# Performance work log

Hardware: AMD Instinct MI355X
Metric: run time of the kernel (lower is better)

Reference implementation:

```python
import jax, jax.numpy as jnp
import numpy as np

I_DIM, K_DIM, V_DIM, O_DIM = 64, 64, 32, 64
P, NH, NK = 7, 2, 4
B, H, W = 8, 256, 256


def get_unfold_params_v2(width, kernel_size, num_kernels):
    # exact replica of the torch helper's search
    if width <= kernel_size:
        return width, 1, 1, 1
    if width <= kernel_size + num_kernels:
        return kernel_size, 1, 1, width - kernel_size + 1

    def _sd(nk):
        d = 1
        while True:
            k = (kernel_size - 1) * d + 1
            if (width - k) % (nk - 1) == 0:
                return (width - k) // (nk - 1), d
            d += 1
            if d >= kernel_size:
                return None, d

    while True:
        s, d = _sd(num_kernels)
        if s and s < (kernel_size - 1) * d + 1:
            return kernel_size, s, d, num_kernels
        num_kernels += 1


def conv1x1(x, Wt, b):
    # x: [B,C,H,W], Wt: [O,C]
    return jnp.einsum('oc,bchw->bohw', Wt, x) + b[None, :, None, None]


def to_patches(x, nh, idx, p):
    # x: [B,C,H,W] -> [B, nh, nph*npw, C//nh, p*p] (unfold + rearrange)
    Bs, C, _, _ = x.shape
    hd = C // nh
    npw = idx.shape[0]
    pt = x[:, :, idx][:, :, :, :, idx]          # [B,C,nph,ph,npw,pw]
    pt = pt.reshape(Bs, nh, hd, npw, p, npw, p)
    pt = pt.transpose(0, 1, 3, 5, 2, 4, 6)       # B,nh,nph,npw,hd,ph,pw
    return pt.reshape(Bs, nh, npw * npw, hd, p * p)


def from_patches(o, nh, idx, p, Hh, Ww):
    # o: [B,nh,S,hd,p*p] -> fold (overlap scatter-add) -> [B, nh*hd, H, W]
    Bs, _, _, hd, _ = o.shape
    npw = idx.shape[0]
    o = o.reshape(Bs, nh, npw, npw, hd, p, p)
    o = o.transpose(0, 1, 4, 2, 5, 3, 6)         # B,nh,hd,nph,ph,npw,pw
    o = o.reshape(Bs, nh * hd, npw, p, npw, p)
    out = jnp.zeros((Bs, nh * hd, Hh, Ww), o.dtype)
    return out.at[:, :, idx[:, :, None, None], idx[None, None, :, :]].add(o)


def setup_inputs() -> dict:
    key = jax.random.key(0)
    ks = jax.random.split(key, 8)
    s = 0.05
    return {
        'x1': jax.random.normal(ks[0], (B, I_DIM, H, W), jnp.float32),
        'x2': jax.random.normal(ks[1], (B, I_DIM, H, W), jnp.float32),
        'Wk': jax.random.normal(ks[2], (2 * K_DIM, I_DIM), jnp.float32) * s,
        'bk': jax.random.normal(ks[3], (2 * K_DIM,), jnp.float32) * s,
        'Wv': jax.random.normal(ks[4], (2 * V_DIM, I_DIM), jnp.float32) * s,
        'bv': jax.random.normal(ks[5], (2 * V_DIM,), jnp.float32) * s,
        'Wp': jax.random.normal(ks[6], (O_DIM, 2 * V_DIM), jnp.float32) * s,
        'bp': jax.random.normal(ks[7], (O_DIM,), jnp.float32) * s,
    }


def reference(x1, x2, Wk, bk, Wv, bv, Wp, bp):
    _, _, Hh, Ww = x1.shape
    p, stride, dilation, nkrn = get_unfold_params_v2(Ww, P, NK)
    idx = np.arange(nkrn)[:, None] * stride + np.arange(p)[None, :] * dilation  # [npw,p]

    # grouped 1x1 convs (groups=2): split weights into per-stream halves
    k1 = conv1x1(x1, Wk[:K_DIM], bk[:K_DIM])
    k2 = conv1x1(x2, Wk[K_DIM:], bk[K_DIM:])
    v1 = conv1x1(x1, Wv[:V_DIM], bv[:V_DIM])
    v2 = conv1x1(x2, Wv[V_DIM:], bv[V_DIM:])

    k1p = to_patches(k1, NH, idx, p)  # [B,nh,S,hd_k,pp]
    k2p = to_patches(k2, NH, idx, p)
    v1p = to_patches(v1, NH, idx, p)  # [B,nh,S,hd_v,pp]
    v2p = to_patches(v2, NH, idx, p)

    scale = k1p.shape[-2] ** (-0.5)
    kk = jnp.einsum('bnsdx,bnsdy->bnsxy', k1p * scale, k2p)  # [B,nh,S,pp,pp]
    a1 = jax.nn.softmax(kk, axis=-2)
    o1 = jnp.einsum('bnsxy,bnsdx->bnsdy', a1, v1p)
    a2 = jax.nn.softmax(kk, axis=-1)
    o2 = jnp.einsum('bnsxy,bnsdy->bnsdx', a2, v2p)

    o1 = from_patches(o1, NH, idx, p, Hh, Ww)  # [B,V_DIM,H,W]
    o2 = from_patches(o2, NH, idx, p, Hh, Ww)
    o = jnp.concatenate([o1, o2], axis=1)      # [B,2*V_DIM,H,W]
    return conv1x1(o, Wp, bp)                  # [B,O_DIM,H,W]
```

## Files before the change

### kernel.cpp

```cpp
#include <hip/hip_runtime.h>

#define BB 8
#define HH 256
#define CIN 64
#define NPW 12
#define SPP 144
#define PP 49
#define PDIM 7
#define STRIDE 21
#define DIL 4
#define NS 84

typedef __attribute__((ext_vector_type(8))) short bf16x8;
typedef __attribute__((ext_vector_type(4))) float f32x4;

#define MFMA(a, b, c) __builtin_amdgcn_mfma_f32_16x16x32_bf16((a), (b), (c), 0, 0, 0)

static __device__ __forceinline__ unsigned short f2bf(float f) {
  union { float f; unsigned u; } v; v.f = f;
  unsigned r = (v.u + 0x7fffu + ((v.u >> 16) & 1u)) >> 16;
  return (unsigned short)r;
}
static __device__ __forceinline__ float bf2f(unsigned short h) {
  union { unsigned u; float f; } v; v.u = ((unsigned)h) << 16;
  return v.f;
}
static __device__ __forceinline__ unsigned pk2(float a, float b) {
  return (unsigned)f2bf(a) | ((unsigned)f2bf(b) << 16);
}
static __device__ __forceinline__ int swz(int col, int row) {
  return ((((col >> 3) ^ (row & 7)) & 7) << 3) | (col & 7);
}

__global__ __launch_bounds__(256, 4) void k1_fused(
    const float* __restrict__ x1, const float* __restrict__ x2,
    const float* __restrict__ Wk, const float* __restrict__ bk,
    const float* __restrict__ Wv, const float* __restrict__ bv,
    const float* __restrict__ Wp, float* __restrict__ P)
{
  __shared__ __align__(16) short lds[20480];

  const int tid = threadIdx.x;
  const int lane = tid & 63;
  const int wid = tid >> 6;
  const int l16 = lane & 15;
  const int l4 = lane >> 4;
  const int blk = blockIdx.x;
  const int b  = blk / SPP;
  const int sp = blk % SPP;
  const int pi = sp / NPW, pj = sp % NPW;
  const int h0 = pi * STRIDE, w0 = pj * STRIDE;

  bf16x8 ahi[3][2], alo[3][2];
  float bias[3][4];
  #pragma unroll
  for (int mi = 0; mi < 3; mi++) {
    const int m = wid * 3 + mi;
    const int r0 = m * 16;
    const int rl = r0 + l16;
    const float* wrow = (r0 < 128) ? (Wk + (size_t)rl * 64)
                                   : (Wv + (size_t)(rl - 128) * 64);
    #pragma unroll
    for (int kt = 0; kt < 2; kt++) {
      const float* wp8 = wrow + kt * 32 + l4 * 8;
      float4 wa = *(const float4*)wp8;
      float4 wb = *(const float4*)(wp8 + 4);
      float wf[8] = {wa.x, wa.y, wa.z, wa.w, wb.x, wb.y, wb.z, wb.w};
      #pragma unroll
      for (int j = 0; j < 8; j++) {
        unsigned short h = f2bf(wf[j]);
        ahi[mi][kt][j] = (short)h;
        alo[mi][kt][j] = (short)f2bf(wf[j] - bf2f(h));
      }
    }
    #pragma unroll
    for (int i = 0; i < 4; i++) {
      int rd = r0 + l4 * 4 + i;
      bias[mi][i] = (r0 < 128) ? bk[rd] : bv[rd - 128];
    }
  }
  float4 wpraw[4];
  {
    const float* wprow = Wp + (size_t)(wid * 16 + l16) * 64;
    #pragma unroll
    for (int kt = 0; kt < 2; kt++) {
      wpraw[kt * 2 + 0] = *(const float4*)(wprow + kt * 32 + l4 * 8);
      wpraw[kt * 2 + 1] = *(const float4*)(wprow + kt * 32 + l4 * 8 + 4);
    }
  }

  for (int i = tid; i < 2 * CIN * PP; i += 256) {
    int src = i / (CIN * PP);
    int r = i - src * (CIN * PP);
    int c = r / PP, t = r - c * PP;
    int ph = t / PDIM, pw = t - ph * PDIM;
    const float* xp = src ? x2 : x1;
    float v = xp[(((size_t)b * CIN + c) * HH + (h0 + ph * DIL)) * HH + (w0 + pw * DIL)];
    lds[(src * 64 + t) * 64 + swz(c, t)] = (short)f2bf(v);
  }
  {
    unsigned* z = (unsigned*)lds;
    for (int i = tid; i < 480; i += 256) { z[1568 + i] = 0u; z[3616 + i] = 0u; }
  }
  __syncthreads();

  {
    #pragma unroll
    for (int mi = 0; mi < 3; mi++) {
      const int m = wid * 3 + mi;
      const int r0 = m * 16;
      const int src = (m < 4) ? 0 : (m < 8 ? 1 : (m < 10 ? 0 : 1));
      #pragma unroll
      for (int nt = 0; nt < 4; nt++) {
        const int t = nt * 16 + l16;
        f32x4 acc = {0.f, 0.f, 0.f, 0.f};
        #pragma unroll
        for (int kt = 0; kt < 2; kt++) {
          bf16x8 xb = *(const bf16x8*)
              &lds[(src * 64 + t) * 64 + ((((kt << 2) + l4) ^ (t & 7)) << 3)];
          acc = MFMA(alo[mi][kt], xb, acc);
          acc = MFMA(ahi[mi][kt], xb, acc);
        }
        if (r0 < 128) {
          const int rcol = r0 + l4 * 4;
          const int base = (rcol < 64) ? 8192 : 12288;
          const int col = rcol & 63;
          unsigned* p = (unsigned*)&lds[base + t * 64 + swz(col, t)];
          p[0] = pk2(acc[0] + bias[mi][0], acc[1] + bias[mi][1]);
          p[1] = pk2(acc[2] + bias[mi][2], acc[3] + bias[mi][3]);
        } else {
          #pragma unroll
          for (int i = 0; i < 4; i++) {
            int rv = r0 - 128 + l4 * 4 + i;
            lds[16384 + rv * 64 + swz(t, rv)] = (short)f2bf(acc[i] + bias[mi][i]);
          }
        }
      }
    }
  }
  __syncthreads();

  const float scale = 0.17677669529663687f;

  {
    const int n = wid >> 1;
    #pragma unroll
    for (int xi = 0; xi < 2; xi++) {
      const int x0 = ((wid & 1) * 2 + xi) * 16;
      const int tA = x0 + l16;
      bf16x8 a = *(const bf16x8*)
          &lds[8192 + tA * 64 + ((((n << 2) + l4) ^ (tA & 7)) << 3)];
      #pragma unroll
      for (int yt = 0; yt < 4; yt++) {
        const int y = yt * 16 + l16;
        bf16x8 bb = *(const bf16x8*)
            &lds[12288 + y * 64 + ((((n << 2) + l4) ^ (y & 7)) << 3)];
        f32x4 acc = {0.f, 0.f, 0.f, 0.f};
        acc = MFMA(a, bb, acc);
        #pragma unroll
        for (int i = 0; i < 4; i++) {
          int x = x0 + l4 * 4 + i;
          lds[(n * 64 + x) * 64 + swz(y, x)] = (short)f2bf(acc[i] * scale);
        }
      }
    }
  }
  __syncthreads();

  {
    float* sStat = (float*)&lds[12288];
    if (tid < 196) {
      int n = tid / 98;
      int r = tid % 98;
      int isRow = r >= 49;
      int j = r - (isRow ? 49 : 0);
      float mx = -1e30f;
      for (int k = 0; k < 49; k++) {
        int xr = isRow ? j : k, yc = isRow ? k : j;
        float v = bf2f((unsigned short)lds[(n * 64 + xr) * 64 + swz(yc, xr)]);
        mx = fmaxf(mx, v);
      }
      float sm = 0.f;
      for (int k = 0; k < 49; k++) {
        int xr = isRow ? j : k, yc = isRow ? k : j;
        float v = bf2f((unsigned short)lds[(n * 64 + xr) * 64 + swz(yc, xr)]);
        sm += __expf(v - mx);
      }
      int kind = isRow ? 2 : 0;
      sStat[(kind * 2 + n) * 64 + j] = mx;
      sStat[((kind + 1) * 2 + n) * 64 + j] = 1.0f / sm;
    }
  }
  __syncthreads();

  {
    const float* sStat = (const float*)&lds[12288];
    const int n = wid >> 1;
    const int side = wid & 1;
    const int rv = side * 32 + n * 16 + l16;
    bf16x8 av[2];
    #pragma unroll
    for (int kt = 0; kt < 2; kt++)
      av[kt] = *(const bf16x8*)
          &lds[16384 + rv * 64 + ((((kt << 2) + l4) ^ (rv & 7)) << 3)];
    if (side == 0) {
      #pragma unroll
      for (int tt = 0; tt < 4; tt++) {
        const int t = tt * 16 + l16;
        const float cm = sStat[(0 * 2 + n) * 64 + t];
        const float cs = sStat[(1 * 2 + n) * 64 + t];
        f32x4 acc = {0.f, 0.f, 0.f, 0.f};
        #pragma unroll
        for (int kt = 0; kt < 2; kt++) {
          bf16x8 bfrag;
          #pragma unroll
          for (int j = 0; j < 8; j++) {
            const int x = kt * 32 + l4 * 8 + j;
            float v = bf2f((unsigned short)lds[(n * 64 + x) * 64 + swz(t, x)]);
            float e = (x < PP) ? __expf(v - cm) : 0.f;
            bfrag[j] = (short)f2bf(e);
          }
          acc = MFMA(av[kt], bfrag, acc);
        }
        const int col = n * 16 + l4 * 4;
        unsigned* p = (unsigned*)&lds[8192 + t * 64 + swz(col, t)];
        p[0] = pk2(acc[0] * cs, acc[1] * cs);
        p[1] = pk2(acc[2] * cs, acc[3] * cs);
      }
    } else {
      #pragma unroll
      for (int xt = 0; xt < 4; xt++) {
        const int x = xt * 16 + l16;
        const float rm = sStat[(2 * 2 + n) * 64 + x];
        const float rs = sStat[(3 * 2 + n) * 64 + x];
        f32x4 acc = {0.f, 0.f, 0.f, 0.f};
        #pragma unroll
        for (int kt = 0; kt < 2; kt++) {
          bf16x8 braw = *(const bf16x8*)
              &lds[(n * 64 + x) * 64 + ((((kt << 2) + l4) ^ (x & 7)) << 3)];
          bf16x8 bfrag;
          #pragma unroll
          for (int j = 0; j < 8; j++) {
            const int y = kt * 32 + l4 * 8 + j;
            float v = bf2f((unsigned short)braw[j]);
            float e = (y < PP) ? __expf(v - rm) : 0.f;
            bfrag[j] = (short)f2bf(e);
          }
          acc = MFMA(av[kt], bfrag, acc);
        }
        const int col = 32 + n * 16 + l4 * 4;
        unsigned* p = (unsigned*)&lds[8192 + x * 64 + swz(col, x)];
        p[0] = pk2(acc[0] * rs, acc[1] * rs);
        p[1] = pk2(acc[2] * rs, acc[3] * rs);
      }
    }
  }
  __syncthreads();

  {
    bf16x8 whi[2], wlo[2];
    #pragma unroll
    for (int kt = 0; kt < 2; kt++) {
      float4 wa = wpraw[kt * 2 + 0];
      float4 wb = wpraw[kt * 2 + 1];
      float wf[8] = {wa.x, wa.y, wa.z, wa.w, wb.x, wb.y, wb.z, wb.w};
      #pragma unroll
      for (int j = 0; j < 8; j++) {
        unsigned short h = f2bf(wf[j]);
        whi[kt][j] = (short)h;
        wlo[kt][j] = (short)f2bf(wf[j] - bf2f(h));
      }
    }
    #pragma unroll
    for (int tt = 0; tt < 4; tt++) {
      const int t = tt * 16 + l16;
      f32x4 acc = {0.f, 0.f, 0.f, 0.f};
      #pragma unroll
      for (int kt = 0; kt < 2; kt++) {
        bf16x8 ob = *(const bf16x8*)
            &lds[8192 + t * 64 + ((((kt << 2) + l4) ^ (t & 7)) << 3)];
        acc = MFMA(wlo[kt], ob, acc);
        acc = MFMA(whi[kt], ob, acc);
      }
      if (t < PP) {
        const int ph = t / 7, pw = t - ph * 7;
        const size_t col = (size_t)(pi * 7 + ph) * NS + (pj * 7 + pw);
        #pragma unroll
        for (int i = 0; i < 4; i++) {
          const int oc = wid * 16 + l4 * 4 + i;
          P[((size_t)b * 64 + oc) * (NS * NS) + col] = acc[i];
        }
      }
    }
  }
}

__global__ __launch_bounds__(256) void k2_merge(
    const float* __restrict__ P, const float* __restrict__ bp,
    float* __restrict__ out)
{
  __shared__ float bps[64];
  __shared__ int wsmap[256];
  const int tid = threadIdx.x;
  const int b = blockIdx.x / HH, h = blockIdx.x % HH;
  if (tid < 64) bps[tid] = bp[tid];
  {
    int w = tid, wsv = -1;
    for (int pj = 0; pj < NPW; pj++) {
      int r = w - pj * STRIDE;
      if (r >= 0 && r <= (PDIM - 1) * DIL && (r % DIL) == 0) { wsv = pj * PDIM + r / DIL; break; }
    }
    wsmap[tid] = wsv;
  }
  int hs = -1;
  for (int pi = 0; pi < NPW; pi++) {
    int r = h - pi * STRIDE;
    if (r >= 0 && r <= (PDIM - 1) * DIL && (r % DIL) == 0) { hs = pi * PDIM + r / DIL; break; }
  }
  __syncthreads();

  const int wq = tid & 63;
  const int ocq = tid >> 6;
  float4* out4 = (float4*)out;

  if (hs < 0) {
    #pragma unroll 4
    for (int oc = ocq; oc < 64; oc += 4) {
      float bv = bps[oc];
      out4[(((size_t)b * 64 + oc) * HH + h) * 64 + wq] = make_float4(bv, bv, bv, bv);
    }
    return;
  }
  const int ws0 = wsmap[wq * 4 + 0], ws1 = wsmap[wq * 4 + 1];
  const int ws2 = wsmap[wq * 4 + 2], ws3 = wsmap[wq * 4 + 3];
  #pragma unroll 4
  for (int oc = ocq; oc < 64; oc += 4) {
    float bv = bps[oc];
    size_t rbase = (((size_t)b * 64 + oc) * NS + hs) * NS;
    float4 v = make_float4(bv, bv, bv, bv);
    if (ws0 >= 0) v.x += P[rbase + ws0];
    if (ws1 >= 0) v.y += P[rbase + ws1];
    if (ws2 >= 0) v.z += P[rbase + ws2];
    if (ws3 >= 0) v.w += P[rbase + ws3];
    out4[(((size_t)b * 64 + oc) * HH + h) * 64 + wq] = v;
  }
}

extern "C" void kernel_launch(void* const* d_in, const int* in_sizes, int n_in,
                              void* d_out, int out_size, void* d_ws, size_t ws_size,
                              hipStream_t stream) {
  const float* x1 = (const float*)d_in[0];
  const float* x2 = (const float*)d_in[1];
  const float* Wk = (const float*)d_in[2];
  const float* bk = (const float*)d_in[3];
  const float* Wv = (const float*)d_in[4];
  const float* bv = (const float*)d_in[5];
  const float* Wp = (const float*)d_in[6];
  const float* bp = (const float*)d_in[7];
  float* P = (float*)d_ws;
  float* out = (float*)d_out;

  k1_fused<<<dim3(BB * SPP), dim3(256), 0, stream>>>(x1, x2, Wk, bk, Wv, bv, Wp, P);
  k2_merge<<<dim3(BB * HH), dim3(256), 0, stream>>>(P, bp, out);
}
```

Baseline: 337.1 us.

## Fuse merge kernel into main kernel, scattering output directly with bias fill

```diff
diff --git a/kernel.cpp b/kernel.cpp
--- a/kernel.cpp
+++ b/kernel.cpp
@@ -31,12 +31,21 @@
 static __device__ __forceinline__ int swz(int col, int row) {
   return ((((col >> 3) ^ (row & 7)) & 7) << 3) | (col & 7);
 }
+static __device__ __forceinline__ int samp_idx(int x) {
+  #pragma unroll
+  for (int pq = 0; pq < NPW; pq++) {
+    int r = x - pq * STRIDE;
+    if (r >= 0 && r <= (PDIM - 1) * DIL && (r % DIL) == 0) return pq * PDIM + r / DIL;
+  }
+  return -1;
+}
 
 __global__ __launch_bounds__(256, 4) void k1_fused(
     const float* __restrict__ x1, const float* __restrict__ x2,
     const float* __restrict__ Wk, const float* __restrict__ bk,
     const float* __restrict__ Wv, const float* __restrict__ bv,
-    const float* __restrict__ Wp, float* __restrict__ P)
+    const float* __restrict__ Wp, const float* __restrict__ bp,
+    float* __restrict__ out)
 {
   __shared__ __align__(16) short lds[20480];
 
@@ -51,6 +60,27 @@
   const int pi = sp / NPW, pj = sp % NPW;
   const int h0 = pi * STRIDE, w0 = pj * STRIDE;
 
+  {
+    float4* out4 = (float4*)out;
+    for (int h = sp; h < HH; h += SPP) {
+      if (samp_idx(h) < 0) {
+        for (int i = tid; i < 64 * 64; i += 256) {
+          int oc = i >> 6, wq = i & 63;
+          float bv0 = bp[oc];
+          out4[(((size_t)b * 64 + oc) * HH + h) * 64 + wq] =
+              make_float4(bv0, bv0, bv0, bv0);
+        }
+      } else {
+        const int w = tid;
+        if (samp_idx(w) < 0) {
+          for (int oc = 0; oc < 64; oc++) {
+            out[(((size_t)b * 64 + oc) * HH + h) * HH + w] = bp[oc];
+          }
+        }
+      }
+    }
+  }
+
   bf16x8 ahi[3][2], alo[3][2];
   float bias[3][4];
   #pragma unroll
@@ -80,6 +110,7 @@
     }
   }
   float4 wpraw[4];
+  float bpv[4];
   {
     const float* wprow = Wp + (size_t)(wid * 16 + l16) * 64;
     #pragma unroll
@@ -87,6 +118,8 @@
       wpraw[kt * 2 + 0] = *(const float4*)(wprow + kt * 32 + l4 * 8);
       wpraw[kt * 2 + 1] = *(const float4*)(wprow + kt * 32 + l4 * 8 + 4);
     }
+    #pragma unroll
+    for (int i = 0; i < 4; i++) bpv[i] = bp[wid * 16 + l4 * 4 + i];
   }
 
   for (int i = tid; i < 2 * CIN * PP; i += 256) {
@@ -284,65 +317,14 @@
       }
       if (t < PP) {
         const int ph = t / 7, pw = t - ph * 7;
-        const size_t col = (size_t)(pi * 7 + ph) * NS + (pj * 7 + pw);
+        const int h = h0 + ph * DIL, w = w0 + pw * DIL;
         #pragma unroll
         for (int i = 0; i < 4; i++) {
           const int oc = wid * 16 + l4 * 4 + i;
-          P[((size_t)b * 64 + oc) * (NS * NS) + col] = acc[i];
-        }
-      }
-    }
-  }
-}
-
-__global__ __launch_bounds__(256) void k2_merge(
-    const float* __restrict__ P, const float* __restrict__ bp,
-    float* __restrict__ out)
-{
-  __shared__ float bps[64];
-  __shared__ int wsmap[256];
-  const int tid = threadIdx.x;
-  const int b = blockIdx.x / HH, h = blockIdx.x % HH;
-  if (tid < 64) bps[tid] = bp[tid];
-  {
-    int w = tid, wsv = -1;
-    for (int pj = 0; pj < NPW; pj++) {
-      int r = w - pj * STRIDE;
-      if (r >= 0 && r <= (PDIM - 1) * DIL && (r % DIL) == 0) { wsv = pj * PDIM + r / DIL; break; }
-    }
-    wsmap[tid] = wsv;
-  }
-  int hs = -1;
-  for (int pi = 0; pi < NPW; pi++) {
-    int r = h - pi * STRIDE;
-    if (r >= 0 && r <= (PDIM - 1) * DIL && (r % DIL) == 0) { hs = pi * PDIM + r / DIL; break; }
-  }
-  __syncthreads();
-
-  const int wq = tid & 63;
-  const int ocq = tid >> 6;
-  float4* out4 = (float4*)out;
-
-  if (hs < 0) {
-    #pragma unroll 4
-    for (int oc = ocq; oc < 64; oc += 4) {
-      float bv = bps[oc];
-      out4[(((size_t)b * 64 + oc) * HH + h) * 64 + wq] = make_float4(bv, bv, bv, bv);
-    }
-    return;
-  }
-  const int ws0 = wsmap[wq * 4 + 0], ws1 = wsmap[wq * 4 + 1];
-  const int ws2 = wsmap[wq * 4 + 2], ws3 = wsmap[wq * 4 + 3];
-  #pragma unroll 4
-  for (int oc = ocq; oc < 64; oc += 4) {
-    float bv = bps[oc];
-    size_t rbase = (((size_t)b * 64 + oc) * NS + hs) * NS;
-    float4 v = make_float4(bv, bv, bv, bv);
-    if (ws0 >= 0) v.x += P[rbase + ws0];
-    if (ws1 >= 0) v.y += P[rbase + ws1];
-    if (ws2 >= 0) v.z += P[rbase + ws2];
-    if (ws3 >= 0) v.w += P[rbase + ws3];
-    out4[(((size_t)b * 64 + oc) * HH + h) * 64 + wq] = v;
+          out[(((size_t)b * 64 + oc) * HH + h) * HH + w] = acc[i] + bpv[i];
+        }
+      }
+    }
   }
 }
 
@@ -357,9 +339,7 @@
   const float* bv = (const float*)d_in[5];
   const float* Wp = (const float*)d_in[6];
   const float* bp = (const float*)d_in[7];
-  float* P = (float*)d_ws;
   float* out = (float*)d_out;
 
-  k1_fused<<<dim3(BB * SPP), dim3(256), 0, stream>>>(x1, x2, Wk, bk, Wv, bv, Wp, P);
-  k2_merge<<<dim3(BB * HH), dim3(256), 0, stream>>>(P, bp, out);
-}
+  k1_fused<<<dim3(BB * SPP), dim3(256), 0, stream>>>(x1, x2, Wk, bk, Wv, bv, Wp, bp, out);
+}
```

After: 345.1 us. 2.4% more time.
